# Optimization experiments

Measured on AMD Instinct MI355X. Metric: run time of the kernel, lower is better.

Reference implementation:

```python
import jax, jax.numpy as jnp
import numpy as np

N, F, H, E = 10000, 256, 256, 320000
TEMPERATURE = 1.0


def setup_inputs() -> dict:
    key = jax.random.key(0)
    k_x, k_ei, k_w1, k_b1, k_w2, k_b2 = jax.random.split(key, 6)
    x = jax.random.normal(k_x, (N, F), dtype=jnp.float32)
    edge_index = jax.random.randint(k_ei, (2, E), 0, N, dtype=jnp.int64)
    # PyTorch nn.Linear default init: U(-1/sqrt(fan_in), 1/sqrt(fan_in)), weight shape (out, in)
    lim1 = 1.0 / np.sqrt(2 * F)
    W1 = jax.random.uniform(k_w1, (H, 2 * F), dtype=jnp.float32, minval=-lim1, maxval=lim1)
    b1 = jax.random.uniform(k_b1, (H,), dtype=jnp.float32, minval=-lim1, maxval=lim1)
    lim2 = 1.0 / np.sqrt(H)
    W2 = jax.random.uniform(k_w2, (1, H), dtype=jnp.float32, minval=-lim2, maxval=lim2)
    b2 = jax.random.uniform(k_b2, (1,), dtype=jnp.float32, minval=-lim2, maxval=lim2)
    return {"x": x, "edge_index": edge_index, "W1": W1, "b1": b1, "W2": W2, "b2": b2}


def reference(x, edge_index, W1, b1, W2, b2):
    row, col = edge_index[0], edge_index[1]
    edge_feat = jnp.concatenate([x[row], x[col]], axis=-1)  # (E, 2F)
    h = jax.nn.relu(edge_feat @ W1.T + b1)                  # (E, H)
    logits = (h @ W2.T + b2).squeeze(-1)                    # (E,)
    m = jax.nn.sigmoid(logits / max(TEMPERATURE, 1e-6))
    return m
```

## Files before the change

### kernel.cpp

```cpp
#include <hip/hip_runtime.h>
#include <hip/hip_bf16.h>


typedef __attribute__((ext_vector_type(8))) short bf16x8;
typedef __attribute__((ext_vector_type(4))) float f32x4;
typedef __attribute__((ext_vector_type(2))) float f32x2;

__device__ __forceinline__ unsigned short f2bf(float f) {
    __hip_bfloat16 h = __float2bfloat16(f);
    return *reinterpret_cast<unsigned short*>(&h);
}

__device__ __forceinline__ unsigned char f2fp8(float f) {
    return (unsigned char)(__builtin_amdgcn_cvt_pk_fp8_f32(f, f, 0, false) & 0xff);
}

__global__ __launch_bounds__(256) void convert_w(const float* __restrict__ w1,
                                                 unsigned short* __restrict__ wb,
                                                 int nw4) {
    int i = blockIdx.x * 256 + threadIdx.x;
    if (i < nw4) {
        float4 v = ((const float4*)w1)[i];
        ushort4 o = {f2bf(v.x), f2bf(v.y), f2bf(v.z), f2bf(v.w)};
        ((ushort4*)wb)[i] = o;
    }
}

__global__ __launch_bounds__(256) void gemm_mfma(const float* __restrict__ x,
                                                 const unsigned short* __restrict__ wb,
                                                 const float* __restrict__ b1,
                                                 unsigned char* __restrict__ uv,
                                                 int M) {
    __shared__ __align__(16) unsigned short As[2][16][40];

    const int t    = threadIdx.x;
    const int wave = t >> 6;
    const int lane = t & 63;
    const int lm   = lane & 15;
    const int lq   = lane >> 4;
    const int lk   = lq * 8;
    const int m0   = blockIdx.x * 16;

    const int srow = t >> 4;
    const int sk   = (t & 15) * 2;
    const int grow = m0 + srow;
    const float* sptr = x + (size_t)(grow < M ? grow : (M - 1)) * 256 + sk;

    const int half    = wave >> 1;
    const int colbase = wave * 128;
    const int rowbase = (wave & 1) * 128;
    const unsigned short* bpre =
        wb + (size_t)(rowbase + lm) * 512 + half * 256 + lk;

    f32x4 acc[8];
#pragma unroll
    for (int j = 0; j < 8; ++j) acc[j] = f32x4{0.f, 0.f, 0.f, 0.f};

    float2 apref = *(const float2*)(sptr);

#pragma unroll
    for (int it = 0; it < 8; ++it) {
        const int kt  = it * 32;
        const int cur = it & 1;
        unsigned int lo = ((unsigned int)f2bf(apref.x));
        unsigned int hi = ((unsigned int)f2bf(apref.y)) << 16;
        *(unsigned int*)&As[cur][srow][sk] = lo | hi;
        if (it < 7) apref = *(const float2*)(sptr + kt + 32);
        __syncthreads();
        bf16x8 a = *(const bf16x8*)&As[cur][lm][lk];
#pragma unroll
        for (int j = 0; j < 8; ++j) {
            bf16x8 b = *(const bf16x8*)(bpre + (size_t)j * 16 * 512 + kt);
            acc[j] = __builtin_amdgcn_mfma_f32_16x16x32_bf16(a, b, acc[j], 0, 0, 0);
        }
    }

    const int row0 = m0 + lq * 4;
#pragma unroll
    for (int j = 0; j < 8; ++j) {
        const int col  = colbase + j * 16 + lm;
        const int cin  = col & 255;
        const float badd = half ? 0.f : b1[cin];
#pragma unroll
        for (int r = 0; r < 4; ++r) {
            if (row0 + r < M)
                uv[(size_t)(row0 + r) * 512 + col] = f2fp8(acc[j][r] + badd);
        }
    }
}

__global__ __launch_bounds__(256) void edge_kernel(const unsigned char* __restrict__ uv,
                                                   const int* __restrict__ ei,
                                                   const float* __restrict__ w2,
                                                   const float* __restrict__ b2p,
                                                   float* __restrict__ out, int E) {
    const int lane = threadIdx.x & 63;
    const int g = lane >> 4;
    const int c = lane & 15;
    const int wid  = (blockIdx.x * blockDim.x + threadIdx.x) >> 6;
    const int nwav = (gridDim.x * blockDim.x) >> 6;
    const int nb   = E >> 2;

    float w2r[16];
#pragma unroll
    for (int i = 0; i < 4; ++i)
        *(float4*)&w2r[i * 4] = *(const float4*)(w2 + c * 16 + i * 4);
    const float b2 = b2p[0];

    for (int b = wid; b < nb; b += 2 * nwav) {
        const int bB = b + nwav;
        const bool has2 = bB < nb;

        const int e0 = b * 4 + g;
        const int r0 = ei[e0];
        const int c0 = ei[E + e0];
        const int e1 = has2 ? bB * 4 + g : e0;
        const int r1 = ei[e1];
        const int c1 = ei[E + e1];

        uint4 ua = *(const uint4*)(uv + (size_t)r0 * 512 + c * 16);
        uint4 va = *(const uint4*)(uv + (size_t)c0 * 512 + 256 + c * 16);
        uint4 ub = *(const uint4*)(uv + (size_t)r1 * 512 + c * 16);
        uint4 vb = *(const uint4*)(uv + (size_t)c1 * 512 + 256 + c * 16);

        unsigned int uw[4], vw[4];
        float p;

        *(uint4*)&uw[0] = ua; *(uint4*)&vw[0] = va;
        {
            float2 p2 = {0.f, 0.f};
#pragma unroll
            for (int w = 0; w < 4; ++w) {
                f32x2 u01 = __builtin_amdgcn_cvt_pk_f32_fp8(uw[w], false);
                f32x2 u23 = __builtin_amdgcn_cvt_pk_f32_fp8(uw[w], true);
                f32x2 v01 = __builtin_amdgcn_cvt_pk_f32_fp8(vw[w], false);
                f32x2 v23 = __builtin_amdgcn_cvt_pk_f32_fp8(vw[w], true);
                float s0 = fmaxf(u01.x + v01.x, 0.f);
                float s1 = fmaxf(u01.y + v01.y, 0.f);
                float s2 = fmaxf(u23.x + v23.x, 0.f);
                float s3 = fmaxf(u23.y + v23.y, 0.f);
                p2.x = fmaf(s0, w2r[4 * w + 0], p2.x);
                p2.y = fmaf(s1, w2r[4 * w + 1], p2.y);
                p2.x = fmaf(s2, w2r[4 * w + 2], p2.x);
                p2.y = fmaf(s3, w2r[4 * w + 3], p2.y);
            }
            p = p2.x + p2.y;
        }
#pragma unroll
        for (int off = 1; off < 16; off <<= 1)
            p += __shfl_xor(p, off, 64);
        if (c == 0) out[e0] = 1.f / (1.f + __expf(-(p + b2)));

        if (has2) {
            *(uint4*)&uw[0] = ub; *(uint4*)&vw[0] = vb;
            float2 p2 = {0.f, 0.f};
#pragma unroll
            for (int w = 0; w < 4; ++w) {
                f32x2 u01 = __builtin_amdgcn_cvt_pk_f32_fp8(uw[w], false);
                f32x2 u23 = __builtin_amdgcn_cvt_pk_f32_fp8(uw[w], true);
                f32x2 v01 = __builtin_amdgcn_cvt_pk_f32_fp8(vw[w], false);
                f32x2 v23 = __builtin_amdgcn_cvt_pk_f32_fp8(vw[w], true);
                float s0 = fmaxf(u01.x + v01.x, 0.f);
                float s1 = fmaxf(u01.y + v01.y, 0.f);
                float s2 = fmaxf(u23.x + v23.x, 0.f);
                float s3 = fmaxf(u23.y + v23.y, 0.f);
                p2.x = fmaf(s0, w2r[4 * w + 0], p2.x);
                p2.y = fmaf(s1, w2r[4 * w + 1], p2.y);
                p2.x = fmaf(s2, w2r[4 * w + 2], p2.x);
                p2.y = fmaf(s3, w2r[4 * w + 3], p2.y);
            }
            p = p2.x + p2.y;
#pragma unroll
            for (int off = 1; off < 16; off <<= 1)
                p += __shfl_xor(p, off, 64);
            if (c == 0) out[e1] = 1.f / (1.f + __expf(-(p + b2)));
        }
    }
}

extern "C" void kernel_launch(void* const* d_in, const int* in_sizes, int n_in,
                              void* d_out, int out_size, void* d_ws, size_t ws_size,
                              hipStream_t stream) {
    const float* x  = (const float*)d_in[0];
    const int*   ei = (const int*)d_in[1];
    const float* W1 = (const float*)d_in[2];
    const float* b1 = (const float*)d_in[3];
    const float* W2 = (const float*)d_in[4];
    const float* b2 = (const float*)d_in[5];
    float* out = (float*)d_out;

    const int N = in_sizes[0] / 256;
    const int E = in_sizes[1] / 2;

    unsigned char*  uv = (unsigned char*)d_ws;
    unsigned short* wb = (unsigned short*)(uv + (size_t)N * 512);

    const int nw4 = (256 * 512) / 4;
    convert_w<<<(nw4 + 255) / 256, 256, 0, stream>>>(W1, wb, nw4);

    gemm_mfma<<<(N + 15) / 16, 256, 0, stream>>>(x, wb, b1, uv, N);

    edge_kernel<<<2048, 256, 0, stream>>>(uv, ei, W2, b2, out, E);
}
```

Baseline: 116.8 us.

## Split GEMM over a second grid dimension and stage full A row tile once

The node GEMM grid gains a second dimension that selects the U or V half, so each block computes 16x256 outputs with 4 accumulators per wave instead of 8. The whole 16x256 bf16 A tile is loaded into shared memory once with one barrier, replacing the per-k-step double-buffered load and sync loop. This doubles block count for more parallelism and removes per-iteration barriers. In exchange, each x row tile is read and converted twice, once per half.

```diff
diff --git a/kernel.cpp b/kernel.cpp
--- a/kernel.cpp
+++ b/kernel.cpp
@@ -31,7 +31,7 @@
                                                  const float* __restrict__ b1,
                                                  unsigned char* __restrict__ uv,
                                                  int M) {
-    __shared__ __align__(16) unsigned short As[2][16][40];
+    __shared__ __align__(16) unsigned short As[16][264];
 
     const int t    = threadIdx.x;
     const int wave = t >> 6;
@@ -40,36 +40,34 @@
     const int lq   = lane >> 4;
     const int lk   = lq * 8;
     const int m0   = blockIdx.x * 16;
-
-    const int srow = t >> 4;
-    const int sk   = (t & 15) * 2;
-    const int grow = m0 + srow;
-    const float* sptr = x + (size_t)(grow < M ? grow : (M - 1)) * 256 + sk;
-
-    const int half    = wave >> 1;
-    const int colbase = wave * 128;
-    const int rowbase = (wave & 1) * 128;
+    const int h    = blockIdx.y;
+
+    {
+        const int srow = t >> 4;
+        const int scol = (t & 15) * 4;
+        const int gr   = m0 + srow;
+        const float* xr = x + (size_t)(gr < M ? gr : (M - 1)) * 256;
+#pragma unroll
+        for (int i = 0; i < 4; ++i) {
+            float4 v = *(const float4*)(xr + scol + i * 64);
+            ushort4 o = {f2bf(v.x), f2bf(v.y), f2bf(v.z), f2bf(v.w)};
+            *(ushort4*)&As[srow][scol + i * 64] = o;
+        }
+    }
+    __syncthreads();
+
     const unsigned short* bpre =
-        wb + (size_t)(rowbase + lm) * 512 + half * 256 + lk;
-
-    f32x4 acc[8];
-#pragma unroll
-    for (int j = 0; j < 8; ++j) acc[j] = f32x4{0.f, 0.f, 0.f, 0.f};
-
-    float2 apref = *(const float2*)(sptr);
-
-#pragma unroll
-    for (int it = 0; it < 8; ++it) {
-        const int kt  = it * 32;
-        const int cur = it & 1;
-        unsigned int lo = ((unsigned int)f2bf(apref.x));
-        unsigned int hi = ((unsigned int)f2bf(apref.y)) << 16;
-        *(unsigned int*)&As[cur][srow][sk] = lo | hi;
-        if (it < 7) apref = *(const float2*)(sptr + kt + 32);
-        __syncthreads();
-        bf16x8 a = *(const bf16x8*)&As[cur][lm][lk];
-#pragma unroll
-        for (int j = 0; j < 8; ++j) {
+        wb + (size_t)(wave * 64 + lm) * 512 + h * 256 + lk;
+
+    f32x4 acc[4];
+#pragma unroll
+    for (int j = 0; j < 4; ++j) acc[j] = f32x4{0.f, 0.f, 0.f, 0.f};
+
+#pragma unroll 4
+    for (int kt = 0; kt < 256; kt += 32) {
+        bf16x8 a = *(const bf16x8*)&As[lm][kt + lk];
+#pragma unroll
+        for (int j = 0; j < 4; ++j) {
             bf16x8 b = *(const bf16x8*)(bpre + (size_t)j * 16 * 512 + kt);
             acc[j] = __builtin_amdgcn_mfma_f32_16x16x32_bf16(a, b, acc[j], 0, 0, 0);
         }
@@ -77,10 +75,10 @@
 
     const int row0 = m0 + lq * 4;
 #pragma unroll
-    for (int j = 0; j < 8; ++j) {
-        const int col  = colbase + j * 16 + lm;
-        const int cin  = col & 255;
-        const float badd = half ? 0.f : b1[cin];
+    for (int j = 0; j < 4; ++j) {
+        const int cin  = wave * 64 + j * 16 + lm;
+        const int col  = h * 256 + cin;
+        const float badd = h ? 0.f : b1[cin];
 #pragma unroll
         for (int r = 0; r < 4; ++r) {
             if (row0 + r < M)
@@ -198,7 +196,8 @@
     const int nw4 = (256 * 512) / 4;
     convert_w<<<(nw4 + 255) / 256, 256, 0, stream>>>(W1, wb, nw4);
 
-    gemm_mfma<<<(N + 15) / 16, 256, 0, stream>>>(x, wb, b1, uv, N);
+    dim3 g((N + 15) / 16, 2);
+    gemm_mfma<<<g, 256, 0, stream>>>(x, wb, b1, uv, N);
 
     edge_kernel<<<2048, 256, 0, stream>>>(uv, ei, W2, b2, out, E);
 }
```

New measurement: 113.8 us. 1.03x faster.
